# Kernel optimization log

Measured on AMD Instinct MI355X. Metric: run time of the kernel, lower is better.

## Reference

```python
import jax, jax.numpy as jnp
import numpy as np

B, N, E, H = 16, 1024, 128, 8  # batch, num_patches, emb_dim, num_heads
INNER = E * H                   # inner_dim = emb_dim * num_heads = 1024
LN_EPS = 1e-5
NEG_MAX = jnp.finfo(jnp.float32).max  # module uses -finfo.max on the diagonal


def setup_inputs() -> dict:
    key = jax.random.key(0)
    k0, k1, k2 = jax.random.split(key, 3)
    x = jax.random.normal(k0, (B, N, E), dtype=jnp.float32)
    ln_w = jnp.ones((E,), jnp.float32)
    ln_b = jnp.zeros((E,), jnp.float32)
    w_qkv = jax.random.normal(k1, (E, 3 * INNER), jnp.float32) * (E ** -0.5)
    scale = jnp.full((H,), E ** -0.5, jnp.float32)  # learnable per-head LSA scale
    w_proj = jax.random.normal(k2, (INNER, E), jnp.float32) * (INNER ** -0.5)
    b_proj = jnp.zeros((E,), jnp.float32)
    return {"x": x, "ln_w": ln_w, "ln_b": ln_b, "w_qkv": w_qkv,
            "scale": scale, "w_proj": w_proj, "b_proj": b_proj}


def reference(x, ln_w, ln_b, w_qkv, scale, w_proj, b_proj):
    # LayerNorm over emb_dim
    mu = jnp.mean(x, axis=-1, keepdims=True)
    var = jnp.mean(jnp.square(x - mu), axis=-1, keepdims=True)
    xn = (x - mu) * jax.lax.rsqrt(var + LN_EPS) * ln_w + ln_b

    # QKV projection (no bias), chunk into q,k,v of [B,N,INNER]
    qkv = xn @ w_qkv
    q, k, v = jnp.split(qkv, 3, axis=-1)

    # 'b n (h d) -> b h n d' with h = H, d = E
    def to_heads(t):
        return t.reshape(B, N, H, E).transpose(0, 2, 1, 3)
    q, k, v = to_heads(q), to_heads(k), to_heads(v)

    # per-head learnable scale (LSA), then mask diagonal to -max
    dots = jnp.einsum("bhnd,bhmd->bhnm", q, k) * scale[None, :, None, None]
    idx = jnp.arange(N)
    dots = dots.at[:, :, idx, idx].set(-NEG_MAX)

    attn = jax.nn.softmax(dots, axis=-1)  # dropout p=0.0 -> identity
    out = jnp.einsum("bhnm,bhmd->bhnd", attn, v)

    # 'b h n d -> b n (h d)', then output projection (with bias)
    out = out.transpose(0, 2, 1, 3).reshape(B, N, INNER)
    return out @ w_proj + b_proj
```

## Files before the change

### kernel.cpp

```cpp
#include <hip/hip_runtime.h>
#include <hip/hip_bf16.h>

typedef __bf16 bf16x8 __attribute__((ext_vector_type(8)));
typedef _Float16 f16x8 __attribute__((ext_vector_type(8)));
typedef float f32x4 __attribute__((ext_vector_type(4)));

__device__ __forceinline__ unsigned short f2bf(float f) {
  union { __hip_bfloat16 h; unsigned short u; } cv;
  cv.h = __float2bfloat16(f);
  return cv.u;
}
__device__ __forceinline__ unsigned short f2h(float f) {
  union { _Float16 h; unsigned short u; } cv;
  cv.h = (_Float16)f;
  return cv.u;
}
__device__ __forceinline__ unsigned int pkrtz(float a, float b) {
  auto h = __builtin_amdgcn_cvt_pkrtz(a, b);
  unsigned int u;
  __builtin_memcpy(&u, &h, 4);
  return u;
}
#if __has_builtin(__builtin_amdgcn_exp2f)
__device__ __forceinline__ float fexp2(float x) { return __builtin_amdgcn_exp2f(x); }
#else
__device__ __forceinline__ float fexp2(float x) { return __expf(0.69314718055994531f * x); }
#endif

__device__ __forceinline__ bf16x8 ld_frag(const unsigned short* p) {
  bf16x8 v;
  __builtin_memcpy(&v, __builtin_assume_aligned(p, 16), 16);
  return v;
}
__device__ __forceinline__ f16x8 ld_f16x8(const unsigned short* p) {
  f16x8 v;
  __builtin_memcpy(&v, __builtin_assume_aligned(p, 16), 16);
  return v;
}
__device__ __forceinline__ uint4 ld16(const unsigned short* p) {
  uint4 v;
  __builtin_memcpy(&v, __builtin_assume_aligned(p, 16), 16);
  return v;
}
__device__ __forceinline__ void st16(unsigned short* p, uint4 v) {
  __builtin_memcpy(__builtin_assume_aligned(p, 16), &v, 16);
}
__device__ __forceinline__ void dma16(const unsigned short* g, unsigned short* l) {
  __builtin_amdgcn_global_load_lds((const __attribute__((address_space(1))) void*)g,
                                   (__attribute__((address_space(3))) void*)l, 16, 0, 0);
}

__global__ __launch_bounds__(256) void ln_kernel(const float* __restrict__ x,
                                                 const float* __restrict__ w,
                                                 const float* __restrict__ b,
                                                 unsigned short* __restrict__ xn) {
  int wave = threadIdx.x >> 6;
  int lane = threadIdx.x & 63;
  int row = blockIdx.x * 4 + wave;
  const float* xr = x + (size_t)row * 128;
  float2 v = *reinterpret_cast<const float2*>(xr + lane * 2);
  float s1 = v.x + v.y;
  float s2 = v.x * v.x + v.y * v.y;
#pragma unroll
  for (int off = 32; off > 0; off >>= 1) {
    s1 += __shfl_xor(s1, off, 64);
    s2 += __shfl_xor(s2, off, 64);
  }
  float mu = s1 * (1.0f / 128.0f);
  float var = s2 * (1.0f / 128.0f) - mu * mu;
  float rstd = rsqrtf(var + 1e-5f);
  float a0 = (v.x - mu) * rstd * w[lane * 2] + b[lane * 2];
  float a1 = (v.y - mu) * rstd * w[lane * 2 + 1] + b[lane * 2 + 1];
  unsigned int pk = (unsigned int)f2bf(a0) | ((unsigned int)f2bf(a1) << 16);
  *reinterpret_cast<unsigned int*>(xn + (size_t)row * 128 + lane * 2) = pk;
}

__global__ __launch_bounds__(256) void tcast_kernel(const float* __restrict__ in,
                                                    unsigned short* __restrict__ out,
                                                    int R, int C) {
  __shared__ float tile[32][33];
  int tx = threadIdx.x & 31, ty = threadIdx.x >> 5;
  int c0 = blockIdx.x * 32, r0 = blockIdx.y * 32;
#pragma unroll
  for (int k = 0; k < 4; k++)
    tile[ty + 8 * k][tx] = in[(size_t)(r0 + ty + 8 * k) * C + c0 + tx];
  __syncthreads();
#pragma unroll
  for (int k = 0; k < 4; k++)
    out[(size_t)(c0 + ty + 8 * k) * R + r0 + tx] = f2bf(tile[tx][ty + 8 * k]);
}

__global__ __launch_bounds__(256) void qkv_gemm(const unsigned short* __restrict__ A,
                                                const unsigned short* __restrict__ Bt,
                                                const float* __restrict__ scale,
                                                unsigned short* __restrict__ qk,
                                                unsigned short* __restrict__ Vt) {
  __shared__ unsigned short Al[128 * 72];
  __shared__ unsigned short Bl[128 * 72];
  int t = threadIdx.x;
  int i0 = blockIdx.x * 128, c0 = blockIdx.y * 128;
  int lg = t & 7, rr = t >> 3;
  int w = t >> 6, lane = t & 63, l15 = lane & 15, quad = lane >> 4;
  int wy = (w >> 1) * 64, wx = (w & 1) * 64;
  const f32x4 fz = {0.f, 0.f, 0.f, 0.f};
  f32x4 acc[4][4];
#pragma unroll
  for (int i = 0; i < 4; i++)
#pragma unroll
    for (int j = 0; j < 4; j++) acc[i][j] = fz;

#pragma unroll
  for (int kt = 0; kt < 2; kt++) {
    int k0 = kt * 64;
    uint4 areg[4], breg[4];
#pragma unroll
    for (int p = 0; p < 4; p++)
      areg[p] = ld16(&A[(size_t)(i0 + rr + 32 * p) * 128 + k0 + lg * 8]);
#pragma unroll
    for (int p = 0; p < 4; p++)
      breg[p] = ld16(&Bt[(size_t)(c0 + rr + 32 * p) * 128 + k0 + lg * 8]);
    __syncthreads();
#pragma unroll
    for (int p = 0; p < 4; p++) st16(&Al[(rr + 32 * p) * 72 + lg * 8], areg[p]);
#pragma unroll
    for (int p = 0; p < 4; p++) st16(&Bl[(rr + 32 * p) * 72 + lg * 8], breg[p]);
    __syncthreads();
#pragma unroll
    for (int ks = 0; ks < 2; ks++) {
      bf16x8 af[4], bfr[4];
#pragma unroll
      for (int i = 0; i < 4; i++)
        af[i] = ld_frag(&Al[(wy + 16 * i + l15) * 72 + 32 * ks + quad * 8]);
#pragma unroll
      for (int j = 0; j < 4; j++)
        bfr[j] = ld_frag(&Bl[(wx + 16 * j + l15) * 72 + 32 * ks + quad * 8]);
#pragma unroll
      for (int i = 0; i < 4; i++)
#pragma unroll
        for (int j = 0; j < 4; j++)
          acc[i][j] = __builtin_amdgcn_mfma_f32_16x16x32_bf16(af[i], bfr[j], acc[i][j], 0, 0, 0);
    }
  }
  if (blockIdx.y < 16) {
    float qsc = (blockIdx.y < 8) ? scale[blockIdx.y] * 1.44269504088896f : 1.0f;
#pragma unroll
    for (int i = 0; i < 4; i++)
#pragma unroll
      for (int j = 0; j < 4; j++)
#pragma unroll
        for (int r = 0; r < 4; r++) {
          int row = i0 + wy + 16 * i + quad * 4 + r;
          int col = c0 + wx + 16 * j + l15;
          qk[(size_t)row * 2048 + col] = f2bf(acc[i][j][r] * qsc);
        }
  } else {
    int vc0 = (blockIdx.y - 16) * 128;
#pragma unroll
    for (int i = 0; i < 4; i++)
#pragma unroll
      for (int j = 0; j < 4; j++) {
        int vcol = vc0 + wx + 16 * j + l15;
        int hh = vcol >> 7, dd = vcol & 127;
        int row0 = i0 + wy + 16 * i + quad * 4;
        int bb = row0 >> 10, nn = row0 & 1023;
        int nnp = (nn & ~31) | (((nn >> 2) & 3) << 3) | (((nn >> 4) & 1) << 2) | (nn & 3);
        ushort4 pk;
        pk.x = f2h(acc[i][j][0]); pk.y = f2h(acc[i][j][1]);
        pk.z = f2h(acc[i][j][2]); pk.w = f2h(acc[i][j][3]);
        *reinterpret_cast<ushort4*>(Vt + (size_t)(bb * 8 + hh) * 131072 +
                                    (size_t)dd * 1024 + nnp) = pk;
      }
  }
}

__global__ __launch_bounds__(512, 2) void attn_kernel(const unsigned short* __restrict__ qk,
                                                      const unsigned short* __restrict__ Vt,
                                                      unsigned short* __restrict__ aout) {
  __shared__ __align__(16) unsigned short Kl[2][64 * 128];
  __shared__ __align__(16) unsigned short Vl[2][128 * 64];
  int t = threadIdx.x;
  int idx = blockIdx.x;
  int bh = idx & 127, qt = idx >> 7;
  int b = bh >> 3, h = bh & 7;
  int q0 = qt * 256;
  int w = t >> 6, lane = t & 63, l15 = lane & 15, quad = lane >> 4;

  bf16x8 qf[2][4];
  {
    const unsigned short* qb = qk + (size_t)(b * 1024) * 2048 + h * 128;
#pragma unroll
    for (int g = 0; g < 2; g++) {
      const unsigned short* qp = qb + (size_t)(q0 + 32 * w + 16 * g + l15) * 2048;
#pragma unroll
      for (int ks = 0; ks < 4; ks++) qf[g][ks] = ld_frag(qp + 32 * ks + quad * 8);
    }
  }
  const f32x4 fz = {0.f, 0.f, 0.f, 0.f};
  f32x4 o[2][8];
#pragma unroll
  for (int g = 0; g < 2; g++)
#pragma unroll
    for (int i = 0; i < 8; i++) o[g][i] = fz;
  float plsum[2] = {0.f, 0.f};

  const unsigned short* kbase = qk + (size_t)(b * 1024) * 2048 + 1024 + h * 128;
  const unsigned short* vbase = Vt + (size_t)bh * 131072;

  int koff[2], voff[2];
#pragma unroll
  for (int i = 0; i < 2; i++) {
    int c = w * 2 + i;
    int krow = c * 4 + (lane >> 4);
    int kg = ((lane & 15) ^ (krow & 7)) * 8;
    koff[i] = krow * 2048 + kg;
    int vrow = c * 8 + (lane >> 3);
    int vg = ((lane & 7) ^ ((vrow >> 1) & 7)) * 8;
    voff[i] = vrow * 1024 + vg;
  }

#pragma unroll
  for (int i = 0; i < 2; i++) {
    dma16(kbase + koff[i], &Kl[0][(w * 2 + i) * 512]);
    dma16(vbase + voff[i], &Vl[0][(w * 2 + i) * 512]);
  }

  for (int kt = 0; kt < 16; kt++) {
    int k0 = kt * 64;
    __syncthreads();
    if (kt < 15) {
      int kn0 = (kt + 1) * 64;
      int nb = (kt + 1) & 1;
#pragma unroll
      for (int i = 0; i < 2; i++) {
        dma16(kbase + (size_t)kn0 * 2048 + koff[i], &Kl[nb][(w * 2 + i) * 512]);
        dma16(vbase + voff[i] + kn0, &Vl[nb][(w * 2 + i) * 512]);
      }
    }
    const unsigned short* Kc = Kl[kt & 1];
    const unsigned short* Vc = Vl[kt & 1];

#pragma unroll
    for (int cp = 0; cp < 2; cp++) {
      f16x8 pa[2];
      {
        unsigned int dw[2][4];
#pragma unroll
        for (int sub = 0; sub < 2; sub++) {
          int ct = cp * 2 + sub;
          f32x4 acc[2] = {fz, fz};
          __builtin_amdgcn_s_setprio(1);
#pragma unroll
          for (int ks = 0; ks < 4; ks++) {
            bf16x8 kf = ld_frag(&Kc[(16 * ct + l15) * 128 + ((4 * ks + quad) ^ (l15 & 7)) * 8]);
#pragma unroll
            for (int g = 0; g < 2; g++)
              acc[g] = __builtin_amdgcn_mfma_f32_16x16x32_bf16(kf, qf[g][ks], acc[g], 0, 0, 0);
          }
          __builtin_amdgcn_s_setprio(0);
#pragma unroll
          for (int g = 0; g < 2; g++) {
            float p[4];
            if ((q0 + 32 * w + 16 * g) == (k0 + 16 * ct)) {
#pragma unroll
              for (int r = 0; r < 4; r++)
                p[r] = ((quad * 4 + r) == l15) ? 0.f : fexp2(acc[g][r]);
            } else {
#pragma unroll
              for (int r = 0; r < 4; r++) p[r] = fexp2(acc[g][r]);
            }
            plsum[g] += (p[0] + p[1]) + (p[2] + p[3]);
            dw[g][sub * 2 + 0] = pkrtz(p[0], p[1]);
            dw[g][sub * 2 + 1] = pkrtz(p[2], p[3]);
          }
        }
#pragma unroll
        for (int g = 0; g < 2; g++) __builtin_memcpy(&pa[g], dw[g], 16);
      }
      __builtin_amdgcn_s_setprio(1);
#pragma unroll
      for (int c8 = 0; c8 < 8; c8++) {
        f16x8 vf = ld_f16x8(&Vc[(16 * c8 + l15) * 64 + ((4 * cp + quad) ^ ((l15 >> 1) & 7)) * 8]);
#pragma unroll
        for (int g = 0; g < 2; g++)
          o[g][c8] = __builtin_amdgcn_mfma_f32_16x16x32_f16(pa[g], vf, o[g][c8], 0, 0, 0);
      }
      __builtin_amdgcn_s_setprio(0);
    }
  }

#pragma unroll
  for (int g = 0; g < 2; g++) {
    float s = plsum[g];
    s += __shfl_xor(s, 16, 64);
    s += __shfl_xor(s, 32, 64);
#pragma unroll
    for (int r = 0; r < 4; r++) {
      float rs = __shfl(s, (lane & 48) + quad * 4 + r, 64);
      float rl = 1.0f / rs;
      int row = b * 1024 + q0 + 32 * w + 16 * g + quad * 4 + r;
#pragma unroll
      for (int c8 = 0; c8 < 8; c8++) {
        int col = h * 128 + 16 * c8 + l15;
        aout[(size_t)row * 1024 + col] = f2bf(o[g][c8][r] * rl);
      }
    }
  }
}

__global__ __launch_bounds__(256) void proj_gemm(const unsigned short* __restrict__ A,
                                                 const unsigned short* __restrict__ Bt,
                                                 const float* __restrict__ bias,
                                                 float* __restrict__ out) {
  __shared__ unsigned short Al[64 * 136];
  __shared__ unsigned short Bl[64 * 136];
  int t = threadIdx.x;
  int i0 = blockIdx.x * 64, c0 = blockIdx.y * 64;
  int w = t >> 6, lane = t & 63, l15 = lane & 15, quad = lane >> 4;
  int wy = (w >> 1) * 32, wx = (w & 1) * 32;
  const f32x4 fz = {0.f, 0.f, 0.f, 0.f};
  f32x4 acc[2][2];
#pragma unroll
  for (int i = 0; i < 2; i++)
#pragma unroll
    for (int j = 0; j < 2; j++) acc[i][j] = fz;
  int l = t & 15, rr = t >> 4;
  for (int kb = 0; kb < 8; kb++) {
    int k0 = kb * 128;
    uint4 areg[4], breg[4];
#pragma unroll
    for (int p = 0; p < 4; p++)
      areg[p] = ld16(&A[(size_t)(i0 + rr + 16 * p) * 1024 + k0 + l * 8]);
#pragma unroll
    for (int p = 0; p < 4; p++)
      breg[p] = ld16(&Bt[(size_t)(c0 + rr + 16 * p) * 1024 + k0 + l * 8]);
    __syncthreads();
#pragma unroll
    for (int p = 0; p < 4; p++) st16(&Al[(rr + 16 * p) * 136 + l * 8], areg[p]);
#pragma unroll
    for (int p = 0; p < 4; p++) st16(&Bl[(rr + 16 * p) * 136 + l * 8], breg[p]);
    __syncthreads();
#pragma unroll
    for (int ks = 0; ks < 4; ks++) {
      bf16x8 af[2], bfr[2];
#pragma unroll
      for (int i = 0; i < 2; i++)
        af[i] = ld_frag(&Al[(wy + 16 * i + l15) * 136 + 32 * ks + quad * 8]);
#pragma unroll
      for (int j = 0; j < 2; j++)
        bfr[j] = ld_frag(&Bl[(wx + 16 * j + l15) * 136 + 32 * ks + quad * 8]);
#pragma unroll
      for (int i = 0; i < 2; i++)
#pragma unroll
        for (int j = 0; j < 2; j++)
          acc[i][j] = __builtin_amdgcn_mfma_f32_16x16x32_bf16(af[i], bfr[j], acc[i][j], 0, 0, 0);
    }
  }
#pragma unroll
  for (int i = 0; i < 2; i++)
#pragma unroll
    for (int j = 0; j < 2; j++) {
      int col = c0 + wx + 16 * j + l15;
      float bv = bias[col];
#pragma unroll
      for (int r = 0; r < 4; r++) {
        int row = i0 + wy + 16 * i + quad * 4 + r;
        out[(size_t)row * 128 + col] = acc[i][j][r] + bv;
      }
    }
}

extern "C" void kernel_launch(void* const* d_in, const int* in_sizes, int n_in,
                              void* d_out, int out_size, void* d_ws, size_t ws_size,
                              hipStream_t stream) {
  const float* x      = (const float*)d_in[0];
  const float* ln_w   = (const float*)d_in[1];
  const float* ln_b   = (const float*)d_in[2];
  const float* w_qkv  = (const float*)d_in[3];
  const float* scale  = (const float*)d_in[4];
  const float* w_proj = (const float*)d_in[5];
  const float* b_proj = (const float*)d_in[6];
  float* out = (float*)d_out;

  char* ws = (char*)d_ws;
  unsigned short* xn     = (unsigned short*)(ws);
  unsigned short* wqkvT  = (unsigned short*)(ws + 4194304);
  unsigned short* wprojT = (unsigned short*)(ws + 4980736);
  unsigned short* qk     = (unsigned short*)(ws + 5242880);
  unsigned short* Vt     = (unsigned short*)(ws + 72351744);
  unsigned short* aout   = (unsigned short*)(ws + 105906176);

  ln_kernel<<<dim3(4096), dim3(256), 0, stream>>>(x, ln_w, ln_b, xn);
  tcast_kernel<<<dim3(96, 4), dim3(256), 0, stream>>>(w_qkv, wqkvT, 128, 3072);
  tcast_kernel<<<dim3(4, 32), dim3(256), 0, stream>>>(w_proj, wprojT, 1024, 128);
  qkv_gemm<<<dim3(128, 24), dim3(256), 0, stream>>>(xn, wqkvT, scale, qk, Vt);
  attn_kernel<<<dim3(512), dim3(512), 0, stream>>>(qk, Vt, aout);
  proj_gemm<<<dim3(256, 2), dim3(256), 0, stream>>>(aout, wprojT, b_proj, out);
}
```

Measured before the change: 194.7 us.

## Use direct-to-LDS DMA loads with XOR swizzle and LDS-staged coalesced QK stores

The QKV GEMM now loads the full K=128 A and B tiles straight into shared memory with dma16 direct-to-LDS copies, using an XOR swizzle instead of padding. This removes the register round-trip and the two-stage k loop with its extra barriers. The Q/K epilogue stages bf16 results in LDS and writes 16-byte coalesced rows in place of scattered 2-byte stores. Shared memory per block grows to 64KB, which may lower occupancy.

```diff
diff --git a/kernel.cpp b/kernel.cpp
--- a/kernel.cpp
+++ b/kernel.cpp
@@ -95,13 +95,24 @@
                                                 const float* __restrict__ scale,
                                                 unsigned short* __restrict__ qk,
                                                 unsigned short* __restrict__ Vt) {
-  __shared__ unsigned short Al[128 * 72];
-  __shared__ unsigned short Bl[128 * 72];
+  __shared__ __align__(16) unsigned short Sm[32768];
+  unsigned short* Al = Sm;
+  unsigned short* Bl = Sm + 16384;
   int t = threadIdx.x;
   int i0 = blockIdx.x * 128, c0 = blockIdx.y * 128;
-  int lg = t & 7, rr = t >> 3;
   int w = t >> 6, lane = t & 63, l15 = lane & 15, quad = lane >> 4;
   int wy = (w >> 1) * 64, wx = (w & 1) * 64;
+
+  {
+    int rrow = (lane >> 4);
+#pragma unroll
+    for (int i = 0; i < 8; i++) {
+      int row = i * 16 + w * 4 + rrow;
+      int gs = (l15 ^ (row & 15)) * 8;
+      dma16(&A[(size_t)(i0 + row) * 128 + gs], &Al[(i * 16 + w * 4) * 128]);
+      dma16(&Bt[(size_t)(c0 + row) * 128 + gs], &Bl[(i * 16 + w * 4) * 128]);
+    }
+  }
   const f32x4 fz = {0.f, 0.f, 0.f, 0.f};
   f32x4 acc[4][4];
 #pragma unroll
@@ -109,50 +120,44 @@
 #pragma unroll
     for (int j = 0; j < 4; j++) acc[i][j] = fz;
 
-#pragma unroll
-  for (int kt = 0; kt < 2; kt++) {
-    int k0 = kt * 64;
-    uint4 areg[4], breg[4];
-#pragma unroll
-    for (int p = 0; p < 4; p++)
-      areg[p] = ld16(&A[(size_t)(i0 + rr + 32 * p) * 128 + k0 + lg * 8]);
-#pragma unroll
-    for (int p = 0; p < 4; p++)
-      breg[p] = ld16(&Bt[(size_t)(c0 + rr + 32 * p) * 128 + k0 + lg * 8]);
-    __syncthreads();
-#pragma unroll
-    for (int p = 0; p < 4; p++) st16(&Al[(rr + 32 * p) * 72 + lg * 8], areg[p]);
-#pragma unroll
-    for (int p = 0; p < 4; p++) st16(&Bl[(rr + 32 * p) * 72 + lg * 8], breg[p]);
-    __syncthreads();
-#pragma unroll
-    for (int ks = 0; ks < 2; ks++) {
-      bf16x8 af[4], bfr[4];
-#pragma unroll
-      for (int i = 0; i < 4; i++)
-        af[i] = ld_frag(&Al[(wy + 16 * i + l15) * 72 + 32 * ks + quad * 8]);
+  __syncthreads();
+
+#pragma unroll
+  for (int ks = 0; ks < 4; ks++) {
+    bf16x8 af[4], bfr[4];
+#pragma unroll
+    for (int i = 0; i < 4; i++)
+      af[i] = ld_frag(&Al[(wy + 16 * i + l15) * 128 + ((4 * ks + quad) ^ l15) * 8]);
+#pragma unroll
+    for (int j = 0; j < 4; j++)
+      bfr[j] = ld_frag(&Bl[(wx + 16 * j + l15) * 128 + ((4 * ks + quad) ^ l15) * 8]);
+#pragma unroll
+    for (int i = 0; i < 4; i++)
 #pragma unroll
       for (int j = 0; j < 4; j++)
-        bfr[j] = ld_frag(&Bl[(wx + 16 * j + l15) * 72 + 32 * ks + quad * 8]);
-#pragma unroll
-      for (int i = 0; i < 4; i++)
-#pragma unroll
-        for (int j = 0; j < 4; j++)
-          acc[i][j] = __builtin_amdgcn_mfma_f32_16x16x32_bf16(af[i], bfr[j], acc[i][j], 0, 0, 0);
-    }
-  }
+        acc[i][j] = __builtin_amdgcn_mfma_f32_16x16x32_bf16(af[i], bfr[j], acc[i][j], 0, 0, 0);
+  }
+
   if (blockIdx.y < 16) {
     float qsc = (blockIdx.y < 8) ? scale[blockIdx.y] * 1.44269504088896f : 1.0f;
+    unsigned short* Cs = Sm;
+    __syncthreads();
 #pragma unroll
     for (int i = 0; i < 4; i++)
 #pragma unroll
       for (int j = 0; j < 4; j++)
 #pragma unroll
-        for (int r = 0; r < 4; r++) {
-          int row = i0 + wy + 16 * i + quad * 4 + r;
-          int col = c0 + wx + 16 * j + l15;
-          qk[(size_t)row * 2048 + col] = f2bf(acc[i][j][r] * qsc);
-        }
+        for (int r = 0; r < 4; r++)
+          Cs[(wy + 16 * i + quad * 4 + r) * 136 + wx + 16 * j + l15] =
+              f2bf(acc[i][j][r] * qsc);
+    __syncthreads();
+    int rr = t >> 4, g8 = (t & 15) * 8;
+#pragma unroll
+    for (int k = 0; k < 8; k++) {
+      int row = k * 16 + rr;
+      uint4 v = ld16(&Cs[row * 136 + g8]);
+      st16(&qk[(size_t)(i0 + row) * 2048 + c0 + g8], v);
+    }
   } else {
     int vc0 = (blockIdx.y - 16) * 128;
 #pragma unroll
```

Result: no change. 195.6 us (+0.5%).
